# Performance work log

Measured on AMD Instinct MI355X. Metric: run time of the kernel, lower is better.

## Reference

```python
import jax, jax.numpy as jnp
import numpy as np

N = 51200      # total nodes
E = 1638400    # total edges (avg degree 32)
G = 512        # graphs in batch
IN = 16        # input node features
H = 4          # heads
C = 32         # channels per head
HC = H * C     # 128, concat output width
SLOPE = 0.2    # LeakyReLU negative slope
BN_EPS = 1e-5


def _glorot(k, shape, fan):
    return jax.random.normal(k, shape, jnp.float32) / np.sqrt(fan).astype(np.float32)


def setup_inputs() -> dict:
    key = jax.random.key(0)
    ks = jax.random.split(key, 32)
    inp = {}
    inp['x'] = jax.random.normal(ks[0], (N, IN), jnp.float32)
    inp['edge_index'] = jax.random.randint(ks[1], (2, E), 0, N)
    inp['batch'] = jnp.sort(jax.random.randint(ks[2], (N,), 0, G))
    # GATv2 layer 1 (IN -> H*C)
    inp['l1_Wl'] = _glorot(ks[3], (IN, HC), IN)
    inp['l1_bl'] = jnp.zeros((HC,), jnp.float32)
    inp['l1_Wr'] = _glorot(ks[4], (IN, HC), IN)
    inp['l1_br'] = jnp.zeros((HC,), jnp.float32)
    inp['l1_att'] = _glorot(ks[5], (H, C), C)
    inp['l1_bias'] = jnp.zeros((HC,), jnp.float32)
    # GATv2 layer 2 (HC -> H*C)
    inp['l2_Wl'] = _glorot(ks[6], (HC, HC), HC)
    inp['l2_bl'] = jnp.zeros((HC,), jnp.float32)
    inp['l2_Wr'] = _glorot(ks[7], (HC, HC), HC)
    inp['l2_br'] = jnp.zeros((HC,), jnp.float32)
    inp['l2_att'] = _glorot(ks[8], (H, C), C)
    inp['l2_bias'] = jnp.zeros((HC,), jnp.float32)
    # MLP head (HC -> HC -> HC -> 2) with BatchNorm (eval mode, running stats 0/1)
    inp['fc1_W'] = _glorot(ks[9], (HC, HC), HC)
    inp['fc1_b'] = jnp.zeros((HC,), jnp.float32)
    inp['bn1_g'] = jnp.ones((HC,), jnp.float32)
    inp['bn1_b'] = jnp.zeros((HC,), jnp.float32)
    inp['fc2_W'] = _glorot(ks[10], (HC, HC), HC)
    inp['fc2_b'] = jnp.zeros((HC,), jnp.float32)
    inp['bn2_g'] = jnp.ones((HC,), jnp.float32)
    inp['bn2_b'] = jnp.zeros((HC,), jnp.float32)
    inp['fc3_W'] = _glorot(ks[11], (HC, 2), HC)
    inp['fc3_b'] = jnp.zeros((2,), jnp.float32)
    return inp


def gatv2_conv(x, src, dst, Wl, bl, Wr, br, att, bias):
    # PyG GATv2Conv (share_weights=False, concat=True), eval mode (no dropout).
    xl = (x @ Wl + bl).reshape(-1, H, C)  # source transform  [N,H,C]
    xr = (x @ Wr + br).reshape(-1, H, C)  # target transform  [N,H,C]
    e = jax.nn.leaky_relu(xl[src] + xr[dst], SLOPE)   # [E,H,C]
    score = jnp.einsum('ehc,hc->eh', e, att)          # [E,H]
    # segment softmax over edges sharing the same target node
    m = jax.ops.segment_max(score, dst, num_segments=N)
    ex = jnp.exp(score - m[dst])
    denom = jax.ops.segment_sum(ex, dst, num_segments=N)
    alpha = ex / (denom[dst] + 1e-16)                 # [E,H]
    out = jax.ops.segment_sum(xl[src] * alpha[:, :, None], dst, num_segments=N)
    return out.reshape(-1, HC) + bias


def reference(x, edge_index, batch,
              l1_Wl, l1_bl, l1_Wr, l1_br, l1_att, l1_bias,
              l2_Wl, l2_bl, l2_Wr, l2_br, l2_att, l2_bias,
              fc1_W, fc1_b, bn1_g, bn1_b,
              fc2_W, fc2_b, bn2_g, bn2_b,
              fc3_W, fc3_b):
    src, dst = edge_index[0], edge_index[1]
    h = jax.nn.relu(gatv2_conv(x, src, dst, l1_Wl, l1_bl, l1_Wr, l1_br, l1_att, l1_bias))
    h = jax.nn.relu(gatv2_conv(h, src, dst, l2_Wl, l2_bl, l2_Wr, l2_br, l2_att, l2_bias))
    # global mean pool over graphs
    s = jax.ops.segment_sum(h, batch, num_segments=G)
    cnt = jax.ops.segment_sum(jnp.ones((N,), h.dtype), batch, num_segments=G)
    g = s / jnp.maximum(cnt, 1.0)[:, None]            # [G,HC]
    # MLP head; BatchNorm1d in eval mode with running_mean=0, running_var=1
    def bn(z, gamma, beta):
        return z * (gamma / np.sqrt(1.0 + BN_EPS).astype(np.float32)) + beta
    g = jax.nn.relu(bn(g @ fc1_W + fc1_b, bn1_g, bn1_b))
    g = jax.nn.relu(bn(g @ fc2_W + fc2_b, bn2_g, bn2_b))
    return g @ fc3_W + fc3_b                          # [G,2]
```

## Files before the change

### kernel.cpp

```cpp
#include <hip/hip_runtime.h>
#include <math.h>

#define NN 51200
#define EE 1638400
#define GG 512
#define INF 16
#define HCC 128
#define NB 400
#define TILE 4096

typedef float vf2 __attribute__((ext_vector_type(2)));
#define FMA2 __builtin_elementwise_fma
#define MIN2 __builtin_elementwise_min
#define MAX2 __builtin_elementwise_max

__global__ __launch_bounds__(256) void k_hist(const int* __restrict__ ei,
                                              int* __restrict__ bcnt) {
    __shared__ int h[NB];
    for (int i = threadIdx.x; i < NB; i += 256) h[i] = 0;
    __syncthreads();
    int e0 = blockIdx.x * TILE;
#pragma unroll
    for (int s = 0; s < 16; s++) {
        int d = ei[EE + e0 + s * 256 + threadIdx.x];
        atomicAdd(&h[d >> 7], 1);
    }
    __syncthreads();
    for (int i = threadIdx.x; i < NB; i += 256)
        if (h[i]) atomicAdd(&bcnt[i], h[i]);
}

__global__ __launch_bounds__(512) void k_scan2(const int* __restrict__ bcnt,
                                               int* __restrict__ bbase,
                                               int* __restrict__ gcur,
                                               int* __restrict__ rowptr) {
    __shared__ int sc[512];
    int t = threadIdx.x;
    int v = (t < NB) ? bcnt[t] : 0;
    sc[t] = v;
    __syncthreads();
    for (int off = 1; off < 512; off <<= 1) {
        int u = (t >= off) ? sc[t - off] : 0;
        __syncthreads();
        sc[t] += u;
        __syncthreads();
    }
    if (t < NB) { int ex = sc[t] - v; bbase[t] = ex; gcur[t] = ex; }
    if (t == 0) { bbase[NB] = EE; rowptr[NN] = EE; }
}

__global__ __launch_bounds__(512) void k_bin(const int* __restrict__ ei,
                                             int* __restrict__ gcur,
                                             uint2* __restrict__ binned) {
    __shared__ int h[512];
    __shared__ int lexcl[NB], lcur[NB], baseg[NB];
    __shared__ uint2 stage[TILE];
    int t = threadIdx.x;
    h[t] = 0;
    __syncthreads();
    int e0 = blockIdx.x * TILE;
    int sv[8], dv[8];
#pragma unroll
    for (int s = 0; s < 8; s++) {
        int e = e0 + s * 512 + t;
        sv[s] = ei[e];
        dv[s] = ei[EE + e];
        atomicAdd(&h[dv[s] >> 7], 1);
    }
    __syncthreads();
    int myh = h[t];
    for (int off = 1; off < 512; off <<= 1) {
        int u = (t >= off) ? h[t - off] : 0;
        __syncthreads();
        h[t] += u;
        __syncthreads();
    }
    if (t < NB) {
        int ex = h[t] - myh;
        lexcl[t] = ex;
        lcur[t] = ex;
        baseg[t] = atomicAdd(&gcur[t], myh);
    }
    __syncthreads();
#pragma unroll
    for (int s = 0; s < 8; s++) {
        int b = dv[s] >> 7;
        int r = atomicAdd(&lcur[b], 1);
        stage[r] = make_uint2((unsigned)sv[s], (unsigned)dv[s]);
    }
    __syncthreads();
#pragma unroll
    for (int s = 0; s < 8; s++) {
        int idx = s * 512 + t;
        uint2 p = stage[idx];
        int b = (int)(p.y >> 7);
        binned[baseg[b] + idx - lexcl[b]] = p;
    }
}

__global__ __launch_bounds__(256) void k_csr(const uint2* __restrict__ binned,
                                             const int* __restrict__ bbase,
                                             int* __restrict__ rowptr,
                                             int* __restrict__ col) {
    int b = blockIdx.x;
    int base = bbase[b];
    int cnt = bbase[b + 1] - base;
    __shared__ int nh[128], ncur[128];
    int t = threadIdx.x;
    if (t < 128) nh[t] = 0;
    __syncthreads();
    for (int e = t; e < cnt; e += 256) {
        uint2 p = binned[base + e];
        atomicAdd(&nh[p.y & 127], 1);
    }
    __syncthreads();
    int myv = (t < 128) ? nh[t] : 0;
    for (int off = 1; off < 128; off <<= 1) {
        int u = (t >= off && t < 128) ? nh[t - off] : 0;
        __syncthreads();
        if (t < 128) nh[t] += u;
        __syncthreads();
    }
    if (t < 128) {
        int ex = nh[t] - myv;
        rowptr[(b << 7) + t] = base + ex;
        ncur[t] = base + ex;
    }
    __syncthreads();
    for (int e = t; e < cnt; e += 256) {
        uint2 p = binned[base + e];
        int r = atomicAdd(&ncur[p.y & 127], 1);
        col[r] = (int)p.x;
    }
}

__global__ __launch_bounds__(256) void k_lin1(const float* __restrict__ x,
                                              const float* __restrict__ Wl,
                                              const float* __restrict__ bl,
                                              const float* __restrict__ Wr,
                                              const float* __restrict__ br,
                                              float* __restrict__ xl,
                                              float* __restrict__ xr) {
    __shared__ float sx[2][INF];
    int j = threadIdx.x & 127;
    int ty = threadIdx.x >> 7;
    int row = blockIdx.x * 2 + ty;
    if (threadIdx.x < 32) {
        int r = blockIdx.x * 2 + (threadIdx.x >> 4);
        sx[threadIdx.x >> 4][threadIdx.x & 15] = x[(size_t)r * INF + (threadIdx.x & 15)];
    }
    __syncthreads();
    float al = bl[j], ar = br[j];
#pragma unroll
    for (int k = 0; k < INF; k++) {
        float xv = sx[ty][k];
        al = fmaf(xv, Wl[k * HCC + j], al);
        ar = fmaf(xv, Wr[k * HCC + j], ar);
    }
    xl[(size_t)row * HCC + j] = al;
    xr[(size_t)row * HCC + j] = ar;
}

#define AST 129
#define BST 260
__global__ __launch_bounds__(512) void k_lin2(const float* __restrict__ hin,
                                              const float* __restrict__ Wl,
                                              const float* __restrict__ bl,
                                              const float* __restrict__ Wr,
                                              const float* __restrict__ br,
                                              float* __restrict__ outl,
                                              float* __restrict__ outr) {
    __shared__ float As[32 * AST];
    __shared__ float Bs[32 * BST];
    const int tid = threadIdx.x;
    const int cx = tid & 31;
    const int cy = tid >> 5;
    const int r0 = blockIdx.x * 128;

    float accL[8][4], accR[8][4];
#pragma unroll
    for (int j = 0; j < 8; j++)
#pragma unroll
        for (int i = 0; i < 4; i++) { accL[j][i] = 0.f; accR[j][i] = 0.f; }

    for (int k0 = 0; k0 < HCC; k0 += 32) {
#pragma unroll
        for (int s = 0; s < 2; s++) {
            int f = tid + 512 * s;
            int row = f >> 3;
            int kk = (f & 7) * 4;
            float4 v = *(const float4*)(hin + (size_t)(r0 + row) * HCC + k0 + kk);
            As[(kk + 0) * AST + row] = v.x;
            As[(kk + 1) * AST + row] = v.y;
            As[(kk + 2) * AST + row] = v.z;
            As[(kk + 3) * AST + row] = v.w;
        }
#pragma unroll
        for (int s = 0; s < 4; s++) {
            int g = tid + 512 * s;
            int kr = g >> 6;
            int c4 = g & 63;
            const float* srcp = (c4 < 32)
                ? (Wl + (size_t)(k0 + kr) * HCC + c4 * 4)
                : (Wr + (size_t)(k0 + kr) * HCC + (c4 - 32) * 4);
            *(float4*)&Bs[kr * BST + c4 * 4] = *(const float4*)srcp;
        }
        __syncthreads();
#pragma unroll 4
        for (int k = 0; k < 32; ++k) {
            float a[8];
#pragma unroll
            for (int j = 0; j < 8; ++j) a[j] = As[k * AST + cy + 16 * j];
            float4 b4l = *(const float4*)&Bs[k * BST + cx * 4];
            float4 b4r = *(const float4*)&Bs[k * BST + 128 + cx * 4];
#pragma unroll
            for (int j = 0; j < 8; ++j) {
                accL[j][0] = fmaf(a[j], b4l.x, accL[j][0]);
                accL[j][1] = fmaf(a[j], b4l.y, accL[j][1]);
                accL[j][2] = fmaf(a[j], b4l.z, accL[j][2]);
                accL[j][3] = fmaf(a[j], b4l.w, accL[j][3]);
                accR[j][0] = fmaf(a[j], b4r.x, accR[j][0]);
                accR[j][1] = fmaf(a[j], b4r.y, accR[j][1]);
                accR[j][2] = fmaf(a[j], b4r.z, accR[j][2]);
                accR[j][3] = fmaf(a[j], b4r.w, accR[j][3]);
            }
        }
        __syncthreads();
    }
    float4 bv_l = *(const float4*)(bl + cx * 4);
    float4 bv_r = *(const float4*)(br + cx * 4);
#pragma unroll
    for (int j = 0; j < 8; ++j) {
        int row = r0 + cy + 16 * j;
        float4 o;
        o.x = accL[j][0] + bv_l.x;
        o.y = accL[j][1] + bv_l.y;
        o.z = accL[j][2] + bv_l.z;
        o.w = accL[j][3] + bv_l.w;
        *(float4*)(outl + (size_t)row * HCC + cx * 4) = o;
        o.x = accR[j][0] + bv_r.x;
        o.y = accR[j][1] + bv_r.y;
        o.z = accR[j][2] + bv_r.z;
        o.w = accR[j][3] + bv_r.w;
        *(float4*)(outr + (size_t)row * HCC + cx * 4) = o;
    }
}

__global__ __launch_bounds__(256) void k_attn(const int* __restrict__ rowptr,
                                              const int* __restrict__ col,
                                              const float* __restrict__ xl,
                                              const float* __restrict__ xr,
                                              const float* __restrict__ att,
                                              const float* __restrict__ bias,
                                              float* __restrict__ hout) {
    const int wave = threadIdx.x >> 6;
    const int lane = threadIdx.x & 63;
    const int sub = lane >> 4;
    const int q = lane & 15;
    const int n = blockIdx.x * 4 + wave;

    const float4 xrv0 = *(const float4*)(xr + (size_t)n * HCC + q * 8);
    const float4 xrv1 = *(const float4*)(xr + (size_t)n * HCC + q * 8 + 4);
    const float4 at0 = *(const float4*)(att + q * 8);
    const float4 at1 = *(const float4*)(att + q * 8 + 4);
    const vf2 xr01 = {xrv0.x, xrv0.y}, xr23 = {xrv0.z, xrv0.w};
    const vf2 xr45 = {xrv1.x, xrv1.y}, xr67 = {xrv1.z, xrv1.w};
    const vf2 at01 = {at0.x, at0.y}, at23 = {at0.z, at0.w};
    const vf2 at45 = {at1.x, at1.y}, at67 = {at1.z, at1.w};
    const vf2 Z2 = {0.f, 0.f}, C2 = {0.2f, 0.2f};
    const unsigned choff = (unsigned)q * 32u;

    const int base = rowptr[n];
    const int deg = rowptr[n + 1] - base;

    float m = -INFINITY, l = 0.f;
    vf2 a01 = Z2, a23 = Z2, a45 = Z2, a67 = Z2;

    for (int i0 = 0; i0 < deg; i0 += 64) {
        int mye = 0;
        if (i0 + lane < deg) mye = col[base + i0 + lane];
        const int cnt = min(64, deg - i0);
        const int groups = (cnt + 15) >> 4;
        for (int g = 0; g < groups; ++g) {
            vf2 v01[4], v23[4], v45[4], v67[4];
#pragma unroll
            for (int k = 0; k < 4; ++k) {
                const int src = __shfl(mye, 16 * g + 4 * k + sub);
                const unsigned voff = ((unsigned)src << 9) + choff;
                const float4 v0 = *(const float4*)((const char*)xl + voff);
                const float4 v1 = *(const float4*)((const char*)xl + voff + 16);
                v01[k] = (vf2){v0.x, v0.y}; v23[k] = (vf2){v0.z, v0.w};
                v45[k] = (vf2){v1.x, v1.y}; v67[k] = (vf2){v1.z, v1.w};
            }
            float p[4];
#pragma unroll
            for (int k = 0; k < 4; ++k) {
                vf2 e, kk, p2;
                e = v01[k] + xr01; kk = FMA2(C2, MIN2(e, Z2), MAX2(e, Z2)); p2 = kk * at01;
                e = v23[k] + xr23; kk = FMA2(C2, MIN2(e, Z2), MAX2(e, Z2)); p2 = FMA2(kk, at23, p2);
                e = v45[k] + xr45; kk = FMA2(C2, MIN2(e, Z2), MAX2(e, Z2)); p2 = FMA2(kk, at45, p2);
                e = v67[k] + xr67; kk = FMA2(C2, MIN2(e, Z2), MAX2(e, Z2)); p2 = FMA2(kk, at67, p2);
                float pp = p2.x + p2.y;
                pp += __shfl_xor(pp, 1);
                pp += __shfl_xor(pp, 2);
                if ((16 * g + 4 * k + sub) >= cnt) pp = -INFINITY;
                p[k] = pp;
            }
            float pm = fmaxf(fmaxf(p[0], p[1]), fmaxf(p[2], p[3]));
            pm = fmaxf(pm, __shfl_xor(pm, 16));
            pm = fmaxf(pm, __shfl_xor(pm, 32));
            const float mn = fmaxf(m, pm);
            const float sc = __expf(m - mn);
            const float w0 = __expf(p[0] - mn);
            const float w1 = __expf(p[1] - mn);
            const float w2 = __expf(p[2] - mn);
            const float w3 = __expf(p[3] - mn);
            l = fmaf(l, sc, (w0 + w1) + (w2 + w3));
            const vf2 S = {sc, sc};
            const vf2 W0 = {w0, w0}, W1 = {w1, w1}, W2 = {w2, w2}, W3 = {w3, w3};
            a01 = FMA2(W3, v01[3], FMA2(W2, v01[2], FMA2(W1, v01[1], FMA2(W0, v01[0], a01 * S))));
            a23 = FMA2(W3, v23[3], FMA2(W2, v23[2], FMA2(W1, v23[1], FMA2(W0, v23[0], a23 * S))));
            a45 = FMA2(W3, v45[3], FMA2(W2, v45[2], FMA2(W1, v45[1], FMA2(W0, v45[0], a45 * S))));
            a67 = FMA2(W3, v67[3], FMA2(W2, v67[2], FMA2(W1, v67[1], FMA2(W0, v67[0], a67 * S))));
            m = mn;
        }
    }
    l += __shfl_xor(l, 16);
    l += __shfl_xor(l, 32);
    float af[8] = {a01.x, a01.y, a23.x, a23.y, a45.x, a45.y, a67.x, a67.y};
#pragma unroll
    for (int i = 0; i < 8; i++) {
        af[i] += __shfl_xor(af[i], 16);
        af[i] += __shfl_xor(af[i], 32);
    }
    const float inv = 1.f / (l + 1e-16f);
    if (sub == 0) {
        const float4 b0 = *(const float4*)(bias + q * 8);
        const float4 b1 = *(const float4*)(bias + q * 8 + 4);
        float4 o0, o1;
        o0.x = fmaxf(fmaf(af[0], inv, b0.x), 0.f);
        o0.y = fmaxf(fmaf(af[1], inv, b0.y), 0.f);
        o0.z = fmaxf(fmaf(af[2], inv, b0.z), 0.f);
        o0.w = fmaxf(fmaf(af[3], inv, b0.w), 0.f);
        o1.x = fmaxf(fmaf(af[4], inv, b1.x), 0.f);
        o1.y = fmaxf(fmaf(af[5], inv, b1.y), 0.f);
        o1.z = fmaxf(fmaf(af[6], inv, b1.z), 0.f);
        o1.w = fmaxf(fmaf(af[7], inv, b1.w), 0.f);
        *(float4*)(hout + (size_t)n * HCC + q * 8) = o0;
        *(float4*)(hout + (size_t)n * HCC + q * 8 + 4) = o1;
    }
}

__global__ __launch_bounds__(128) void k_head(const float* __restrict__ h,
                                              const int* __restrict__ batch,
                                              const float* __restrict__ fc1W, const float* __restrict__ fc1b,
                                              const float* __restrict__ bn1g, const float* __restrict__ bn1b,
                                              const float* __restrict__ fc2W, const float* __restrict__ fc2b,
                                              const float* __restrict__ bn2g, const float* __restrict__ bn2b,
                                              const float* __restrict__ fc3W, const float* __restrict__ fc3b,
                                              float* __restrict__ out) {
    int g = blockIdx.x;
    int j = threadIdx.x;
    __shared__ float buf[HCC], buf2[HCC];
    int lo = 0, hi = NN;
    while (lo < hi) { int mid = (lo + hi) >> 1; if (batch[mid] < g) lo = mid + 1; else hi = mid; }
    int s = lo;
    lo = 0; hi = NN;
    while (lo < hi) { int mid = (lo + hi) >> 1; if (batch[mid] < g + 1) lo = mid + 1; else hi = mid; }
    int e = lo;
    float sum = 0.f;
    for (int n = s; n < e; n++) sum += h[(size_t)n * HCC + j];
    float cnt = (float)(e - s);
    buf[j] = sum / fmaxf(cnt, 1.0f);
    __syncthreads();
    const float SQ = 1.00000499998749994f;
    float a = fc1b[j];
    for (int k = 0; k < HCC; k++) a = fmaf(buf[k], fc1W[k * HCC + j], a);
    a = fmaf(a, bn1g[j] / SQ, bn1b[j]);
    a = fmaxf(a, 0.f);
    buf2[j] = a;
    __syncthreads();
    a = fc2b[j];
    for (int k = 0; k < HCC; k++) a = fmaf(buf2[k], fc2W[k * HCC + j], a);
    a = fmaf(a, bn2g[j] / SQ, bn2b[j]);
    a = fmaxf(a, 0.f);
    buf[j] = a;
    __syncthreads();
    if (j < 2) {
        float o = fc3b[j];
        for (int k = 0; k < HCC; k++) o = fmaf(buf[k], fc3W[k * 2 + j], o);
        out[g * 2 + j] = o;
    }
}

extern "C" void kernel_launch(void* const* d_in, const int* in_sizes, int n_in,
                              void* d_out, int out_size, void* d_ws, size_t ws_size,
                              hipStream_t stream) {
    const float* x      = (const float*)d_in[0];
    const int*   ei     = (const int*)d_in[1];
    const int*   batch  = (const int*)d_in[2];
    const float* l1_Wl  = (const float*)d_in[3];
    const float* l1_bl  = (const float*)d_in[4];
    const float* l1_Wr  = (const float*)d_in[5];
    const float* l1_br  = (const float*)d_in[6];
    const float* l1_att = (const float*)d_in[7];
    const float* l1_bias= (const float*)d_in[8];
    const float* l2_Wl  = (const float*)d_in[9];
    const float* l2_bl  = (const float*)d_in[10];
    const float* l2_Wr  = (const float*)d_in[11];
    const float* l2_br  = (const float*)d_in[12];
    const float* l2_att = (const float*)d_in[13];
    const float* l2_bias= (const float*)d_in[14];
    const float* fc1_W  = (const float*)d_in[15];
    const float* fc1_b  = (const float*)d_in[16];
    const float* bn1_g  = (const float*)d_in[17];
    const float* bn1_b  = (const float*)d_in[18];
    const float* fc2_W  = (const float*)d_in[19];
    const float* fc2_b  = (const float*)d_in[20];
    const float* bn2_g  = (const float*)d_in[21];
    const float* bn2_b  = (const float*)d_in[22];
    const float* fc3_W  = (const float*)d_in[23];
    const float* fc3_b  = (const float*)d_in[24];
    float* out = (float*)d_out;

    float* xl = (float*)d_ws;
    float* xr = xl + (size_t)NN * HCC;
    float* h  = xr + (size_t)NN * HCC;
    int* rowptr = (int*)(h + (size_t)NN * HCC);
    int* col    = rowptr + (NN + 1);
    int* bcnt   = col + EE;
    int* bbase  = bcnt + NB;
    int* gcur   = bbase + (NB + 1);
    uint2* binned = (uint2*)xl;

    hipMemsetAsync(bcnt, 0, NB * sizeof(int), stream);
    k_hist<<<EE / TILE, 256, 0, stream>>>(ei, bcnt);
    k_scan2<<<1, 512, 0, stream>>>(bcnt, bbase, gcur, rowptr);
    k_bin<<<EE / TILE, 512, 0, stream>>>(ei, gcur, binned);
    k_csr<<<NB, 256, 0, stream>>>(binned, bbase, rowptr, col);

    k_lin1<<<NN / 2, 256, 0, stream>>>(x, l1_Wl, l1_bl, l1_Wr, l1_br, xl, xr);
    k_attn<<<NN / 4, 256, 0, stream>>>(rowptr, col, xl, xr, l1_att, l1_bias, h);

    k_lin2<<<NN / 128, 512, 0, stream>>>(h, l2_Wl, l2_bl, l2_Wr, l2_br, xl, xr);
    k_attn<<<NN / 4, 256, 0, stream>>>(rowptr, col, xl, xr, l2_att, l2_bias, h);

    k_head<<<GG, 128, 0, stream>>>(h, batch, fc1_W, fc1_b, bn1_g, bn1_b,
                                   fc2_W, fc2_b, bn2_g, bn2_b, fc3_W, fc3_b, out);
}
```

Before: 511.4 us.

## Pack binned edges into 32-bit words and permute xl/xr channel layout

Binned edge pairs are packed as src | dst<<16 in one 32-bit word instead of a uint2. This halves the staging, shared-memory and global traffic in k_bin and k_csr, and relies on N fitting in 16 bits. Separately, k_lin1 and k_lin2 write xl/xr in a permuted column order. Each attention lane's two float4 loads then fall into two contiguous 256-byte half-rows rather than adjacent 16-byte pairs, which is meant to improve coalescing of the gathered neighbor features. The risk is that the layout must stay consistent across writers and readers.

```diff
diff --git a/kernel.cpp b/kernel.cpp
--- a/kernel.cpp
+++ b/kernel.cpp
@@ -13,6 +13,7 @@
 #define FMA2 __builtin_elementwise_fma
 #define MIN2 __builtin_elementwise_min
 #define MAX2 __builtin_elementwise_max
+
 
 __global__ __launch_bounds__(256) void k_hist(const int* __restrict__ ei,
                                               int* __restrict__ bcnt) {
@@ -51,10 +52,10 @@
 
 __global__ __launch_bounds__(512) void k_bin(const int* __restrict__ ei,
                                              int* __restrict__ gcur,
-                                             uint2* __restrict__ binned) {
+                                             unsigned* __restrict__ binned) {
     __shared__ int h[512];
     __shared__ int lexcl[NB], lcur[NB], baseg[NB];
-    __shared__ uint2 stage[TILE];
+    __shared__ unsigned stage[TILE];
     int t = threadIdx.x;
     h[t] = 0;
     __syncthreads();
@@ -86,19 +87,19 @@
     for (int s = 0; s < 8; s++) {
         int b = dv[s] >> 7;
         int r = atomicAdd(&lcur[b], 1);
-        stage[r] = make_uint2((unsigned)sv[s], (unsigned)dv[s]);
+        stage[r] = (unsigned)sv[s] | ((unsigned)dv[s] << 16);
     }
     __syncthreads();
 #pragma unroll
     for (int s = 0; s < 8; s++) {
         int idx = s * 512 + t;
-        uint2 p = stage[idx];
-        int b = (int)(p.y >> 7);
+        unsigned p = stage[idx];
+        int b = (int)(p >> 23);
         binned[baseg[b] + idx - lexcl[b]] = p;
     }
 }
 
-__global__ __launch_bounds__(256) void k_csr(const uint2* __restrict__ binned,
+__global__ __launch_bounds__(256) void k_csr(const unsigned* __restrict__ binned,
                                              const int* __restrict__ bbase,
                                              int* __restrict__ rowptr,
                                              int* __restrict__ col) {
@@ -110,8 +111,8 @@
     if (t < 128) nh[t] = 0;
     __syncthreads();
     for (int e = t; e < cnt; e += 256) {
-        uint2 p = binned[base + e];
-        atomicAdd(&nh[p.y & 127], 1);
+        unsigned p = binned[base + e];
+        atomicAdd(&nh[(p >> 16) & 127], 1);
     }
     __syncthreads();
     int myv = (t < 128) ? nh[t] : 0;
@@ -128,9 +129,9 @@
     }
     __syncthreads();
     for (int e = t; e < cnt; e += 256) {
-        uint2 p = binned[base + e];
-        int r = atomicAdd(&ncur[p.y & 127], 1);
-        col[r] = (int)p.x;
+        unsigned p = binned[base + e];
+        int r = atomicAdd(&ncur[(p >> 16) & 127], 1);
+        col[r] = (int)(p & 0xFFFFu);
     }
 }
 
@@ -157,8 +158,9 @@
         al = fmaf(xv, Wl[k * HCC + j], al);
         ar = fmaf(xv, Wr[k * HCC + j], ar);
     }
-    xl[(size_t)row * HCC + j] = al;
-    xr[(size_t)row * HCC + j] = ar;
+    int s = 64 * ((j >> 2) & 1) + 4 * (j >> 3) + (j & 3);
+    xl[(size_t)row * HCC + s] = al;
+    xr[(size_t)row * HCC + s] = ar;
 }
 
 #define AST 129
@@ -229,6 +231,7 @@
     }
     float4 bv_l = *(const float4*)(bl + cx * 4);
     float4 bv_r = *(const float4*)(br + cx * 4);
+    const int soff = 64 * (cx & 1) + (cx >> 1) * 4;
 #pragma unroll
     for (int j = 0; j < 8; ++j) {
         int row = r0 + cy + 16 * j;
@@ -237,12 +240,12 @@
         o.y = accL[j][1] + bv_l.y;
         o.z = accL[j][2] + bv_l.z;
         o.w = accL[j][3] + bv_l.w;
-        *(float4*)(outl + (size_t)row * HCC + cx * 4) = o;
+        *(float4*)(outl + (size_t)row * HCC + soff) = o;
         o.x = accR[j][0] + bv_r.x;
         o.y = accR[j][1] + bv_r.y;
         o.z = accR[j][2] + bv_r.z;
         o.w = accR[j][3] + bv_r.w;
-        *(float4*)(outr + (size_t)row * HCC + cx * 4) = o;
+        *(float4*)(outr + (size_t)row * HCC + soff) = o;
     }
 }
 
@@ -259,8 +262,8 @@
     const int q = lane & 15;
     const int n = blockIdx.x * 4 + wave;
 
-    const float4 xrv0 = *(const float4*)(xr + (size_t)n * HCC + q * 8);
-    const float4 xrv1 = *(const float4*)(xr + (size_t)n * HCC + q * 8 + 4);
+    const float4 xrv0 = *(const float4*)(xr + (size_t)n * HCC + q * 4);
+    const float4 xrv1 = *(const float4*)(xr + (size_t)n * HCC + 64 + q * 4);
     const float4 at0 = *(const float4*)(att + q * 8);
     const float4 at1 = *(const float4*)(att + q * 8 + 4);
     const vf2 xr01 = {xrv0.x, xrv0.y}, xr23 = {xrv0.z, xrv0.w};
@@ -268,7 +271,7 @@
     const vf2 at01 = {at0.x, at0.y}, at23 = {at0.z, at0.w};
     const vf2 at45 = {at1.x, at1.y}, at67 = {at1.z, at1.w};
     const vf2 Z2 = {0.f, 0.f}, C2 = {0.2f, 0.2f};
-    const unsigned choff = (unsigned)q * 32u;
+    const unsigned choff = (unsigned)q * 16u;
 
     const int base = rowptr[n];
     const int deg = rowptr[n + 1] - base;
@@ -288,7 +291,7 @@
                 const int src = __shfl(mye, 16 * g + 4 * k + sub);
                 const unsigned voff = ((unsigned)src << 9) + choff;
                 const float4 v0 = *(const float4*)((const char*)xl + voff);
-                const float4 v1 = *(const float4*)((const char*)xl + voff + 16);
+                const float4 v1 = *(const float4*)((const char*)xl + voff + 256);
                 v01[k] = (vf2){v0.x, v0.y}; v23[k] = (vf2){v0.z, v0.w};
                 v45[k] = (vf2){v1.x, v1.y}; v67[k] = (vf2){v1.z, v1.w};
             }
@@ -431,7 +434,7 @@
     int* bcnt   = col + EE;
     int* bbase  = bcnt + NB;
     int* gcur   = bbase + (NB + 1);
-    uint2* binned = (uint2*)xl;
+    unsigned* binned = (unsigned*)xl;
 
     hipMemsetAsync(bcnt, 0, NB * sizeof(int), stream);
     k_hist<<<EE / TILE, 256, 0, stream>>>(ei, bcnt);
```

After: 516.4 us. About the same (+1.0%).
